# Kernel tuning notes

Hardware: AMD Instinct MI355X
Metric: run time of the kernel (lower is better)

Reference implementation:

```python
import jax, jax.numpy as jnp
import numpy as np

K = 16  # neighbors


def _knn_indices(coords, k):
    # coords: (B, 3, N) -> indices (B, N, k) of k nearest points (incl. self)
    sq = jnp.sum(coords * coords, axis=1)                      # (B, N)
    d2 = sq[:, :, None] + sq[:, None, :] - 2.0 * jnp.einsum('bcn,bcm->bnm', coords, coords)
    _, idx = jax.lax.top_k(-d2, k)                             # smallest distances
    return idx


def _gather(points, idx):
    # points: (B, C, N), idx: (B, N, k) -> (B, C, N, k)
    return jax.vmap(lambda p, i: p[:, i])(points, idx)


def setup_inputs() -> dict:
    key = jax.random.key(0)
    ks = jax.random.split(key, 8)
    B, N, C_IN, C_OUT = 4, 8192, 64, 64
    s = 0.05
    return {
        'features': jax.random.normal(ks[0], (B, C_IN, N), dtype=jnp.float32),
        'coords': jax.random.normal(ks[1], (B, 3, N), dtype=jnp.float32),
        'w_lin': jax.random.normal(ks[2], (3 * C_OUT, C_IN), dtype=jnp.float32) * s,
        'w_theta1': jax.random.normal(ks[3], (C_OUT, 3), dtype=jnp.float32) * s,
        'w_theta2': jax.random.normal(ks[4], (C_OUT, C_OUT), dtype=jnp.float32) * s,
        'w_gamma1': jax.random.normal(ks[5], (C_OUT, C_OUT), dtype=jnp.float32) * s,
        'w_gamma2': jax.random.normal(ks[6], (C_OUT, C_OUT), dtype=jnp.float32) * s,
    }


def reference(features, coords, w_lin, w_theta1, w_theta2, w_gamma1, w_gamma2):
    # KNN (int indices, non-differentiable)
    idx = _knn_indices(coords, K)                              # (B, N, k)

    knn_coords = _gather(coords, idx)                          # (B, 3, N, k)
    rel = coords[:, :, :, None] - knn_coords                   # localize * -1
    delta = jnp.einsum('oc,bcnk->bonk', w_theta1, rel)
    delta = jax.nn.relu(jnp.einsum('oc,bcnk->bonk', w_theta2, delta))  # (B, Co, N, k)

    # input linear -> phi, psi, alpha
    feat3 = jnp.einsum('oc,bcn->bon', w_lin, features)         # (B, 3*Co, N)
    phi, psi, alpha = jnp.split(feat3, 3, axis=1)

    psi_g = _gather(psi, idx)                                  # (B, Co, N, k)
    inputs_gamma = phi[:, :, :, None] - psi_g + delta          # localize*-1 + delta
    g = jnp.einsum('oc,bcnk->bonk', w_gamma1, inputs_gamma)
    g = jax.nn.relu(jnp.einsum('oc,bcnk->bonk', w_gamma2, g))
    rho = jax.nn.softmax(g, axis=-1)                           # softmax over k

    alpha_g = _gather(alpha, idx) + delta                      # (B, Co, N, k)
    return jnp.sum(rho * alpha_g, axis=-1)                     # (B, Co, N)
```

## Files before the change

### kernel.cpp

```cpp
#include <hip/hip_runtime.h>
#include <cstdint>


#define NPT 8192
typedef unsigned long long u64;
typedef unsigned int u32;
typedef unsigned short u16;
typedef __attribute__((ext_vector_type(8))) short bf8_t;
typedef __attribute__((ext_vector_type(4))) float f32x4;

__device__ __forceinline__ u16 f2bf(float x) {
  return (u16)((__float_as_uint(x) + 0x8000u) >> 16);
}
__device__ __forceinline__ u32 pkbf(float lo, float hi) {
  return (u32)f2bf(lo) | ((u32)f2bf(hi) << 16);
}
__device__ __forceinline__ float bf2f(u16 v) {
  return __uint_as_float((u32)v << 16);
}
__device__ __forceinline__ u32 med3u(u32 a, u32 b, u32 c) {
  u32 d;
  asm("v_med3_u32 %0, %1, %2, %3" : "=v"(d) : "v"(a), "v"(b), "v"(c));
  return d;
}
__device__ __forceinline__ u32 add3u(u32 a, u32 b, u32 c) {
  u32 d;
  asm("v_add3_u32 %0, %1, %2, %3" : "=v"(d) : "v"(a), "v"(b), "v"(c));
  return d;
}
__device__ __forceinline__ u32 wave_min_u32(u32 v) {
  u32 t;
  t = (u32)__builtin_amdgcn_update_dpp((int)v, (int)v, 0x111, 0xF, 0xF, false); v = min(v, t);
  t = (u32)__builtin_amdgcn_update_dpp((int)v, (int)v, 0x112, 0xF, 0xF, false); v = min(v, t);
  t = (u32)__builtin_amdgcn_update_dpp((int)v, (int)v, 0x114, 0xF, 0xF, false); v = min(v, t);
  t = (u32)__builtin_amdgcn_update_dpp((int)v, (int)v, 0x118, 0xF, 0xF, false); v = min(v, t);
  t = (u32)__builtin_amdgcn_update_dpp((int)v, (int)v, 0x142, 0xF, 0xF, false); v = min(v, t);
  t = (u32)__builtin_amdgcn_update_dpp((int)v, (int)v, 0x143, 0xF, 0xF, false); v = min(v, t);
  return (u32)__builtin_amdgcn_readlane((int)v, 63);
}
__device__ __forceinline__ void lds_cp16(float4* lds_dst, const float4* gsrc) {
  __builtin_amdgcn_global_load_lds(
      (const __attribute__((address_space(1))) unsigned int*)(const void*)gsrc,
      (__attribute__((address_space(3))) unsigned int*)(void*)lds_dst, 16, 0, 0);
}

__global__ __launch_bounds__(256) void fold1_k(
    const float* __restrict__ wg1, const float* __restrict__ wg2,
    const float* __restrict__ wt1, const float* __restrict__ wt2,
    float* __restrict__ G, float* __restrict__ Mrow, float* __restrict__ McT) {
  int t = blockIdx.x * 256 + threadIdx.x;
  if (t < 4096) {
    int o = t >> 6, c = t & 63;
    float acc = 0.f;
    for (int cp = 0; cp < 64; ++cp) acc = fmaf(wg2[o * 64 + cp], wg1[cp * 64 + c], acc);
    G[o * 64 + c] = acc;
  } else if (t < 4096 + 192) {
    int i = t - 4096;
    int o = i / 3, j = i - o * 3;
    float acc = 0.f;
    for (int c = 0; c < 64; ++c) acc = fmaf(wt2[o * 64 + c], wt1[c * 3 + j], acc);
    Mrow[o * 3 + j] = acc;
    McT[j * 64 + o] = acc;
  }
}

__global__ __launch_bounds__(256) void fold2_k(
    const float* __restrict__ G, const float* __restrict__ wl,
    u16* __restrict__ GF, u16* __restrict__ WF) {
  int t = blockIdx.x * 256 + threadIdx.x;
  if (t < 12288) {
    int o = t >> 6, c = t & 63;
    float acc = 0.f;
    if (o < 64) {
      for (int cp = 0; cp < 64; ++cp) acc = fmaf(G[o * 64 + cp], wl[cp * 64 + c], acc);
    } else if (o < 128) {
      for (int cp = 0; cp < 64; ++cp) acc = fmaf(G[(o - 64) * 64 + cp], wl[(64 + cp) * 64 + c], acc);
    } else {
      acc = wl[o * 64 + c];
    }
    int ot = o >> 4, m = o & 15;
    int kh = c >> 5, q = (c >> 3) & 3, j = c & 7;
    WF[(((ot * 2 + kh) * 64) + (q * 16 + m)) * 8 + j] = f2bf(acc);
  } else {
    int i = t - 12288;
    int o = i >> 6, c = i & 63;
    int ot = o >> 4, m = o & 15;
    int kh = c >> 5, q = (c >> 3) & 3, j = c & 7;
    GF[(((ot * 2 + kh) * 64) + (q * 16 + m)) * 8 + j] = f2bf(G[o * 64 + c]);
  }
}

__global__ __launch_bounds__(256) void pack_k(const float* __restrict__ coords,
                                              float4* __restrict__ pack) {
  int g = blockIdx.x * 256 + threadIdx.x;
  int b = g >> 13, n = g & (NPT - 1);
  const float* c = coords + (size_t)b * 3 * NPT;
  float x = c[n], y = c[NPT + n], z = c[2 * NPT + n];
  float sq = __fadd_rn(__fadd_rn(__fmul_rn(x, x), __fmul_rn(y, y)), __fmul_rn(z, z));
  pack[g] = make_float4(x, y, z, sq);
}

#define QPB 8
#define CHUNK 1024
#define NQ 32768
__global__ __launch_bounds__(512) void knn_k(const float4* __restrict__ pack,
                                             u32* __restrict__ part) {
  __shared__ float4 C[2][CHUNK];
  int tid = threadIdx.x;
  int w = tid >> 6, lane = tid & 63;
  int query = blockIdx.x * QPB + w;
  int b = query >> 13, n = query & (NPT - 1);
  const float4* pk = pack + (size_t)b * NPT;
  float4 q = pk[n];
  float qsq = q.w;
  u32 arr[8];
#pragma unroll
  for (int j = 0; j < 8; ++j) arr[j] = 0xFFFFFFFFu;
  lds_cp16(&C[0][tid], pk + tid);
  lds_cp16(&C[0][512 + tid], pk + 512 + tid);
  __syncthreads();
  for (int c0 = 0; c0 < NPT; c0 += CHUNK) {
    int cur = (c0 >> 10) & 1;
    if (c0 + CHUNK < NPT) {
      lds_cp16(&C[cur ^ 1][tid], pk + (c0 + CHUNK) + tid);
      lds_cp16(&C[cur ^ 1][512 + tid], pk + (c0 + CHUNK) + 512 + tid);
    }
    u32 ibase = (u32)(c0 + lane);
#pragma unroll 4
    for (int t = 0; t < CHUNK / 64; ++t) {
      float4 c4 = C[cur][t * 64 + lane];
      float dot = fmaf(q.z, c4.z, fmaf(q.y, c4.y, q.x * c4.x));
      float d2 = fmaxf(fmaf(-2.f, dot, qsq + c4.w), 0.f);
      u32 key = add3u(__float_as_uint(d2) & 0xFFFFE000u, ibase, (u32)(t * 64));
      arr[7] = med3u(key, arr[6], arr[7]);
      arr[6] = med3u(key, arr[5], arr[6]);
      arr[5] = med3u(key, arr[4], arr[5]);
      arr[4] = med3u(key, arr[3], arr[4]);
      arr[3] = med3u(key, arr[2], arr[3]);
      arr[2] = med3u(key, arr[1], arr[2]);
      arr[1] = med3u(key, arr[0], arr[1]);
      arr[0] = min(arr[0], key);
    }
    __syncthreads();
  }
  u32 mg = 0xFFFFFFFFu;
#pragma unroll 1
  for (int r = 0; r < 24; ++r) {
    u32 m = wave_min_u32(arr[0]);
    if (lane == r) mg = m;
    if (arr[0] == m) {
      arr[0] = arr[1]; arr[1] = arr[2]; arr[2] = arr[3]; arr[3] = arr[4];
      arr[4] = arr[5]; arr[5] = arr[6]; arr[6] = arr[7]; arr[7] = 0xFFFFFFFFu;
    }
  }
  if (lane < 24) part[(size_t)lane * NQ + query] = mg;
}

__global__ __launch_bounds__(64) void refine_k(const float4* __restrict__ pack,
                                               const u32* __restrict__ part,
                                               int* __restrict__ idxk) {
  int g = blockIdx.x * 64 + threadIdx.x;
  int b = g >> 13;
  const float4* pk = pack + (size_t)b * NPT;
  float4 q = pk[g & (NPT - 1)];
  float qx = q.x, qy = q.y, qz = q.z, qs = q.w;
  float bd[16];
  int bi[16];
#pragma unroll
  for (int j = 0; j < 16; ++j) { bd[j] = 1e30f; bi[j] = 0x7FFFFFFF; }
#pragma unroll 4
  for (int j = 0; j < 24; ++j) {
    int m = (int)(part[(size_t)j * NQ + g] & 0x1FFFu);
    float4 pm = pk[m];
    float dot = __fadd_rn(__fadd_rn(__fmul_rn(qx, pm.x), __fmul_rn(qy, pm.y)),
                          __fmul_rn(qz, pm.z));
    float kd = __fsub_rn(__fadd_rn(qs, pm.w), __fmul_rn(2.0f, dot));
    int ki = m;
    if (kd < bd[15] || (kd == bd[15] && ki < bi[15])) {
#pragma unroll
      for (int qq = 0; qq < 16; ++qq) {
        bool cs = (kd < bd[qq]) || (kd == bd[qq] && ki < bi[qq]);
        float td = bd[qq];
        int ti = bi[qq];
        bd[qq] = cs ? kd : td;
        bi[qq] = cs ? ki : ti;
        kd = cs ? td : kd;
        ki = cs ? ti : ki;
      }
    }
  }
#pragma unroll
  for (int j = 0; j < 16; ++j) idxk[(size_t)g * 16 + j] = bi[j];
}

__global__ __launch_bounds__(256) void feat_k(const float* __restrict__ features,
                                              const u16* __restrict__ WF,
                                              float* __restrict__ featA,
                                              u16* __restrict__ featB) {
  int tid = threadIdx.x;
  int w = tid >> 6, l = tid & 63;
  int quad = l >> 4, col = l & 15;
  int P = blockIdx.x * 64 + w * 16 + col;
  int b = P >> 13, n = P & (NPT - 1);
  const float* fb = features + (size_t)b * 64 * NPT + n;
  const bf8_t* wfr = (const bf8_t*)WF;
  bf8_t Bf[2];
#pragma unroll
  for (int kh = 0; kh < 2; ++kh) {
    union { u32 wv[4]; bf8_t v; } ub;
#pragma unroll
    for (int j2 = 0; j2 < 4; ++j2) {
      float lo = fb[(size_t)(kh * 32 + quad * 8 + j2 * 2) * NPT];
      float hi = fb[(size_t)(kh * 32 + quad * 8 + j2 * 2 + 1) * NPT];
      ub.wv[j2] = pkbf(lo, hi);
    }
    Bf[kh] = ub.v;
  }
#pragma unroll
  for (int ot = 0; ot < 12; ++ot) {
    bf8_t A0 = wfr[(ot * 2 + 0) * 64 + l];
    bf8_t A1 = wfr[(ot * 2 + 1) * 64 + l];
    f32x4 acc = {0.f, 0.f, 0.f, 0.f};
    acc = __builtin_amdgcn_mfma_f32_16x16x32_bf16(A0, Bf[0], acc, 0, 0, 0);
    acc = __builtin_amdgcn_mfma_f32_16x16x32_bf16(A1, Bf[1], acc, 0, 0, 0);
    int gr = ot * 16 + quad * 4;
    if (ot < 4) {
      *(float4*)(featA + (size_t)P * 64 + gr) = make_float4(acc[0], acc[1], acc[2], acc[3]);
    } else {
      uint2 wv2 = make_uint2(pkbf(acc[0], acc[1]), pkbf(acc[2], acc[3]));
      *(uint2*)(featB + (size_t)P * 128 + (gr - 64)) = wv2;
    }
  }
}

#define SROW 68
__global__ __launch_bounds__(64) void attn_k(
    const float4* __restrict__ pack, const int* __restrict__ idxk,
    const float* __restrict__ featA, const u16* __restrict__ featB,
    const u16* __restrict__ GF, const float* __restrict__ Mrow,
    const float* __restrict__ McT, float* __restrict__ out) {
  __shared__ u16 S16[64 * SROW];
  int l = threadIdx.x;
  int quad = l >> 4, col = l & 15;
  int Pb = blockIdx.x * 4;
  int b = Pb >> 13;
  int nb0 = Pb & (NPT - 1);
  const float4* pkb = pack + (size_t)b * NPT;
  int idxv = idxk[(size_t)Pb * 16 + l];
  int mve[4];
#pragma unroll
  for (int t = 0; t < 4; ++t) mve[t] = __shfl(idxv, t * 16 + col);
  float relx[4], rely[4], relz[4];
#pragma unroll
  for (int t = 0; t < 4; ++t) {
    float4 own = pkb[nb0 + t];
    float4 nbr = pkb[mve[t]];
    relx[t] = own.x - nbr.x; rely[t] = own.y - nbr.y; relz[t] = own.z - nbr.z;
  }
  bf8_t Bf[4][2];
#pragma unroll
  for (int kh = 0; kh < 2; ++kh) {
    const float* mr = Mrow + (kh * 32 + quad * 8) * 3;
    float m_[24];
#pragma unroll
    for (int i6 = 0; i6 < 6; ++i6) {
      float4 v = *(const float4*)(mr + i6 * 4);
      m_[i6 * 4] = v.x; m_[i6 * 4 + 1] = v.y; m_[i6 * 4 + 2] = v.z; m_[i6 * 4 + 3] = v.w;
    }
#pragma unroll
    for (int t = 0; t < 4; ++t) {
      float u_[8];
#pragma unroll
      for (int j = 0; j < 8; ++j)
        u_[j] = fmaxf(fmaf(m_[j * 3 + 2], relz[t],
                           fmaf(m_[j * 3 + 1], rely[t], m_[j * 3] * relx[t])), 0.f);
      union { u32 w[4]; bf8_t v; } ub;
#pragma unroll
      for (int j2 = 0; j2 < 4; ++j2) ub.w[j2] = pkbf(u_[j2 * 2], u_[j2 * 2 + 1]);
      Bf[t][kh] = ub.v;
    }
  }
  const bf8_t* gfr = (const bf8_t*)GF;
#pragma unroll
  for (int ot = 0; ot < 4; ++ot) {
    bf8_t A0 = gfr[(ot * 2 + 0) * 64 + l];
    bf8_t A1 = gfr[(ot * 2 + 1) * 64 + l];
#pragma unroll
    for (int pt = 0; pt < 4; ++pt) {
      f32x4 acc = {0.f, 0.f, 0.f, 0.f};
      acc = __builtin_amdgcn_mfma_f32_16x16x32_bf16(A0, Bf[pt][0], acc, 0, 0, 0);
      acc = __builtin_amdgcn_mfma_f32_16x16x32_bf16(A1, Bf[pt][1], acc, 0, 0, 0);
      const float* phn = featA + (size_t)(Pb + pt) * 64 + ot * 16 + quad * 4;
      float4 ph = *(const float4*)phn;
      uint2 psw = *(const uint2*)(featB + ((size_t)b * NPT + mve[pt]) * 128 + ot * 16 + quad * 4);
      float g0 = fmaxf(acc[0] + ph.x - bf2f((u16)(psw.x & 0xFFFF)), 0.f);
      float g1 = fmaxf(acc[1] + ph.y - bf2f((u16)(psw.x >> 16)), 0.f);
      float g2 = fmaxf(acc[2] + ph.z - bf2f((u16)(psw.y & 0xFFFF)), 0.f);
      float g3 = fmaxf(acc[3] + ph.w - bf2f((u16)(psw.y >> 16)), 0.f);
      uint2 wv = make_uint2(pkbf(g0, g1), pkbf(g2, g3));
      *(uint2*)&S16[(pt * 16 + col) * SROW + ot * 16 + quad * 4] = wv;
    }
  }
  __syncthreads();
  float mc0 = McT[l], mc1 = McT[64 + l], mc2 = McT[128 + l];
  float accv[4];
#pragma unroll 1
  for (int pj = 0; pj < 4; ++pj) {
    float4 ownq = pkb[nb0 + pj];
    float gvv[16];
    float mx = -1e30f;
#pragma unroll
    for (int r = 0; r < 16; ++r) {
      gvv[r] = bf2f(S16[(pj * 16 + r) * SROW + l]);
      mx = fmaxf(mx, gvv[r]);
    }
    float s = 0.f;
#pragma unroll
    for (int r = 0; r < 16; ++r) {
      float e = __expf(gvv[r] - mx);
      gvv[r] = e;
      s += e;
    }
    float inv = 1.0f / s;
    float acc = 0.f;
#pragma unroll
    for (int r = 0; r < 16; ++r) {
      int si = __builtin_amdgcn_readlane(idxv, pj * 16 + r);
      float dl = fmaxf(fmaf(mc2, ownq.z - pkb[si].z,
                            fmaf(mc1, ownq.y - pkb[si].y, mc0 * (ownq.x - pkb[si].x))), 0.f);
      float al = bf2f(featB[((size_t)b * NPT + si) * 128 + 64 + l]);
      acc = fmaf(gvv[r] * inv, al + dl, acc);
    }
    accv[pj] = acc;
  }
  *(float4*)(out + ((size_t)b * 64 + l) * NPT + nb0) =
      make_float4(accv[0], accv[1], accv[2], accv[3]);
}

extern "C" void kernel_launch(void* const* d_in, const int* in_sizes, int n_in,
                              void* d_out, int out_size, void* d_ws, size_t ws_size,
                              hipStream_t stream) {
  const float* features = (const float*)d_in[0];
  const float* coords = (const float*)d_in[1];
  const float* w_lin = (const float*)d_in[2];
  const float* w_t1 = (const float*)d_in[3];
  const float* w_t2 = (const float*)d_in[4];
  const float* w_g1 = (const float*)d_in[5];
  const float* w_g2 = (const float*)d_in[6];
  float* out = (float*)d_out;
  char* ws = (char*)d_ws;
  float4* pack = (float4*)ws;
  float* G = (float*)(ws + 524288);
  float* Mrow = (float*)(ws + 540672);
  float* McT = (float*)(ws + 541440);
  int* idxk = (int*)(ws + 591360);
  float* featA = (float*)(ws + 2688512);
  u16* featB = (u16*)(ws + 11077120);
  u32* part = (u32*)(ws + 2688512);
  u16* GF = (u16*)(ws + 19465728);
  u16* WF = (u16*)(ws + 19473920);

  fold1_k<<<17, 256, 0, stream>>>(w_g1, w_g2, w_t1, w_t2, G, Mrow, McT);
  fold2_k<<<64, 256, 0, stream>>>(G, w_lin, GF, WF);
  pack_k<<<128, 256, 0, stream>>>(coords, pack);
  knn_k<<<4096, 512, 0, stream>>>(pack, part);
  refine_k<<<512, 64, 0, stream>>>(pack, part, idxk);
  feat_k<<<512, 256, 0, stream>>>(features, WF, featA, featB);
  attn_k<<<8192, 64, 0, stream>>>(pack, idxk, featA, featB, GF, Mrow, McT, out);
}
```

Baseline: 274.6 us.

## Process four queries per wave in KNN to reuse LDS candidate loads

Each wave in the KNN kernel now handles four queries instead of one. Every candidate point read from LDS is scored against all four queries, and the query coordinates are made wave-uniform with readfirstlane so they can sit in scalar registers. The grid shrinks fourfold, which cuts the number of global-to-LDS chunk copies and LDS reads per query. In exchange each lane holds 32 sorted-key registers instead of 8, raising register pressure and possibly lowering occupancy, and the unroll factor drops from 4 to 2.

```diff
diff --git a/kernel.cpp b/kernel.cpp
--- a/kernel.cpp
+++ b/kernel.cpp
@@ -23,10 +23,8 @@
   asm("v_med3_u32 %0, %1, %2, %3" : "=v"(d) : "v"(a), "v"(b), "v"(c));
   return d;
 }
-__device__ __forceinline__ u32 add3u(u32 a, u32 b, u32 c) {
-  u32 d;
-  asm("v_add3_u32 %0, %1, %2, %3" : "=v"(d) : "v"(a), "v"(b), "v"(c));
-  return d;
+__device__ __forceinline__ float rfl_f(float x) {
+  return __uint_as_float((u32)__builtin_amdgcn_readfirstlane((int)__float_as_uint(x)));
 }
 __device__ __forceinline__ u32 wave_min_u32(u32 v) {
   u32 t;
@@ -100,7 +98,7 @@
   pack[g] = make_float4(x, y, z, sq);
 }
 
-#define QPB 8
+#define QW 4
 #define CHUNK 1024
 #define NQ 32768
 __global__ __launch_bounds__(512) void knn_k(const float4* __restrict__ pack,
@@ -108,14 +106,21 @@
   __shared__ float4 C[2][CHUNK];
   int tid = threadIdx.x;
   int w = tid >> 6, lane = tid & 63;
-  int query = blockIdx.x * QPB + w;
-  int b = query >> 13, n = query & (NPT - 1);
+  int q0 = blockIdx.x * 32 + w * QW;
+  int b = q0 >> 13, n0 = q0 & (NPT - 1);
   const float4* pk = pack + (size_t)b * NPT;
-  float4 q = pk[n];
-  float qsq = q.w;
-  u32 arr[8];
-#pragma unroll
-  for (int j = 0; j < 8; ++j) arr[j] = 0xFFFFFFFFu;
+  float qx[QW], qy[QW], qz[QW], qs[QW];
+#pragma unroll
+  for (int j = 0; j < QW; ++j) {
+    float4 qv = pk[n0 + j];
+    qx[j] = rfl_f(qv.x); qy[j] = rfl_f(qv.y);
+    qz[j] = rfl_f(qv.z); qs[j] = rfl_f(qv.w);
+  }
+  u32 arr[QW][8];
+#pragma unroll
+  for (int j = 0; j < QW; ++j)
+#pragma unroll
+    for (int s = 0; s < 8; ++s) arr[j][s] = 0xFFFFFFFFu;
   lds_cp16(&C[0][tid], pk + tid);
   lds_cp16(&C[0][512 + tid], pk + 512 + tid);
   __syncthreads();
@@ -125,35 +130,43 @@
       lds_cp16(&C[cur ^ 1][tid], pk + (c0 + CHUNK) + tid);
       lds_cp16(&C[cur ^ 1][512 + tid], pk + (c0 + CHUNK) + 512 + tid);
     }
-    u32 ibase = (u32)(c0 + lane);
-#pragma unroll 4
+#pragma unroll 2
     for (int t = 0; t < CHUNK / 64; ++t) {
       float4 c4 = C[cur][t * 64 + lane];
-      float dot = fmaf(q.z, c4.z, fmaf(q.y, c4.y, q.x * c4.x));
-      float d2 = fmaxf(fmaf(-2.f, dot, qsq + c4.w), 0.f);
-      u32 key = add3u(__float_as_uint(d2) & 0xFFFFE000u, ibase, (u32)(t * 64));
-      arr[7] = med3u(key, arr[6], arr[7]);
-      arr[6] = med3u(key, arr[5], arr[6]);
-      arr[5] = med3u(key, arr[4], arr[5]);
-      arr[4] = med3u(key, arr[3], arr[4]);
-      arr[3] = med3u(key, arr[2], arr[3]);
-      arr[2] = med3u(key, arr[1], arr[2]);
-      arr[1] = med3u(key, arr[0], arr[1]);
-      arr[0] = min(arr[0], key);
+      u32 ib = (u32)(c0 + t * 64) + (u32)lane;
+#pragma unroll
+      for (int j = 0; j < QW; ++j) {
+        float dot = fmaf(qz[j], c4.z, fmaf(qy[j], c4.y, qx[j] * c4.x));
+        float d2 = fmaxf(fmaf(-2.f, dot, qs[j] + c4.w), 0.f);
+        u32 key = (__float_as_uint(d2) & 0xFFFFE000u) + ib;
+        arr[j][7] = med3u(key, arr[j][6], arr[j][7]);
+        arr[j][6] = med3u(key, arr[j][5], arr[j][6]);
+        arr[j][5] = med3u(key, arr[j][4], arr[j][5]);
+        arr[j][4] = med3u(key, arr[j][3], arr[j][4]);
+        arr[j][3] = med3u(key, arr[j][2], arr[j][3]);
+        arr[j][2] = med3u(key, arr[j][1], arr[j][2]);
+        arr[j][1] = med3u(key, arr[j][0], arr[j][1]);
+        arr[j][0] = min(arr[j][0], key);
+      }
     }
     __syncthreads();
   }
-  u32 mg = 0xFFFFFFFFu;
+#pragma unroll
+  for (int j = 0; j < QW; ++j) {
+    u32 mg = 0xFFFFFFFFu;
 #pragma unroll 1
-  for (int r = 0; r < 24; ++r) {
-    u32 m = wave_min_u32(arr[0]);
-    if (lane == r) mg = m;
-    if (arr[0] == m) {
-      arr[0] = arr[1]; arr[1] = arr[2]; arr[2] = arr[3]; arr[3] = arr[4];
-      arr[4] = arr[5]; arr[5] = arr[6]; arr[6] = arr[7]; arr[7] = 0xFFFFFFFFu;
-    }
-  }
-  if (lane < 24) part[(size_t)lane * NQ + query] = mg;
+    for (int r = 0; r < 24; ++r) {
+      u32 m = wave_min_u32(arr[j][0]);
+      if (lane == r) mg = m;
+      if (arr[j][0] == m) {
+        arr[j][0] = arr[j][1]; arr[j][1] = arr[j][2];
+        arr[j][2] = arr[j][3]; arr[j][3] = arr[j][4];
+        arr[j][4] = arr[j][5]; arr[j][5] = arr[j][6];
+        arr[j][6] = arr[j][7]; arr[j][7] = 0xFFFFFFFFu;
+      }
+    }
+    if (lane < 24) part[(size_t)lane * NQ + q0 + j] = mg;
+  }
 }
 
 __global__ __launch_bounds__(64) void refine_k(const float4* __restrict__ pack,
@@ -363,7 +376,7 @@
   fold1_k<<<17, 256, 0, stream>>>(w_g1, w_g2, w_t1, w_t2, G, Mrow, McT);
   fold2_k<<<64, 256, 0, stream>>>(G, w_lin, GF, WF);
   pack_k<<<128, 256, 0, stream>>>(coords, pack);
-  knn_k<<<4096, 512, 0, stream>>>(pack, part);
+  knn_k<<<1024, 512, 0, stream>>>(pack, part);
   refine_k<<<512, 64, 0, stream>>>(pack, part, idxk);
   feat_k<<<512, 256, 0, stream>>>(features, WF, featA, featB);
   attn_k<<<8192, 64, 0, stream>>>(pack, idxk, featA, featB, GF, Mrow, McT, out);
```

After: 276.3 us. No clear change (+0.6%).
